# Optimization experiments

Hardware: AMD Instinct MI355X
Metric: run time of the kernel (lower is better)

Reference implementation:

```python
import jax, jax.numpy as jnp
import numpy as np
from jax import lax

N_ITERS = 20  # fixed-point iterations for the competitive-binding solve


def setup_inputs() -> dict:
    key = jax.random.key(0)
    k1, k2, k3 = jax.random.split(key, 3)
    B, nA, nB, nY = 16384, 64, 64, 1
    AT = jax.random.uniform(k1, (B, nA), dtype=jnp.float32)          # total concentrations, positive
    K_raw = jax.random.normal(k2, (nA, nB), dtype=jnp.float32)        # raw param; effective K = clamp(exp(K_raw),0,1e3)
    BT_raw = jnp.zeros((nB,), dtype=jnp.float32)                      # exp(0)=1 matches module's BT init
    W_raw = jax.random.normal(k3, (nY, nA * nB), dtype=jnp.float32)
    b_raw = jnp.zeros((nY,), dtype=jnp.float32)
    return {"AT": AT, "K_raw": K_raw, "BT_raw": BT_raw, "W_raw": W_raw, "b_raw": b_raw}


def reference(AT, K_raw, BT_raw, W_raw, b_raw):
    # parametrizations: ExpConstrain then ClampConstrain(0,1000)
    K = jnp.clip(jnp.exp(K_raw), 0.0, 1000.0)        # (nA,nB)
    BT = jnp.clip(jnp.exp(BT_raw), 0.0, 1000.0)      # (nB,)
    B = AT.shape[0]
    ATe = AT[:, :, None]                              # (B,nA,1)
    BTe = BT[None, None, :]                           # (1,1,nB), broadcasts over batch

    def one_iter(AF):
        BF = BTe / ((K * AF).sum(axis=1, keepdims=True) + 1.0)   # (B,1,nB)
        return ATe / ((K * BF).sum(axis=2, keepdims=True) + 1.0) # (B,nA,1)

    # fixed-point solve (solvers.torch_solve equivalent)
    AF = lax.fori_loop(0, N_ITERS, lambda i, a: one_iter(a), ATe)

    # mode == 'comp': extra refinement steps as written in forward
    BF = BTe / ((K * AF).sum(axis=1, keepdims=True) + 1.0)
    AF = ATe / ((K * BF).sum(axis=2, keepdims=True) + 1.0)
    BF = BTe / ((K * AF).sum(axis=1, keepdims=True) + 1.0)
    C = AF * BF * K                                   # (B,nA,nB)

    H = C.reshape(B, -1)                              # output == 'C'
    W = jnp.clip(W_raw, -10.0, 10.0)                  # linear_constrain == 'none'
    b = jnp.clip(b_raw, -10.0, 10.0)
    Y = H @ W.T + b                                   # (B,1)
    return jnp.squeeze(Y, axis=1)                     # (B,)
```

## Files before the change

### kernel.cpp

```cpp
#include <hip/hip_runtime.h>
#include <stdint.h>


typedef __attribute__((ext_vector_type(8))) short s8v;
typedef __attribute__((ext_vector_type(4))) float f4v;
typedef __attribute__((ext_vector_type(4))) unsigned u4v;

#define NPAIR 21

__device__ __forceinline__ unsigned cvtpk(float lo, float hi) {
    unsigned r;
    asm("v_cvt_pk_bf16_f32 %0, %1, %2" : "=v"(r) : "v"(lo), "v"(hi));
    return r;
}
__device__ __forceinline__ void swap32(unsigned& a, unsigned& b) {
    asm("v_permlane32_swap_b32 %0, %1" : "+v"(a), "+v"(b));
}
__device__ __forceinline__ void swap16(unsigned& a, unsigned& b) {
    asm("v_permlane16_swap_b32 %0, %1" : "+v"(a), "+v"(b));
}
__device__ __forceinline__ float clipexp(float x) {
    return fminf(__expf(x), 1000.f);
}
__device__ __forceinline__ float wclip(float x) {
    return fminf(fmaxf(x, -10.f), 10.f);
}

union FragU { unsigned u[4]; s8v s; u4v v; };

__device__ __forceinline__ s8v packB(f4v va, f4v vb) {
    unsigned a0 = cvtpk(va[0], va[1]), a1 = cvtpk(va[2], va[3]);
    unsigned b0 = cvtpk(vb[0], vb[1]), b1 = cvtpk(vb[2], vb[3]);
    swap32(a0, b0); swap16(a0, b0);
    swap32(a1, b1); swap16(a1, b1);
    FragU U; U.u[0] = a0; U.u[1] = a1; U.u[2] = b0; U.u[3] = b1;
    return U.s;
}

__global__ __launch_bounds__(64, 1)
void cn_main(const float* __restrict__ AT,
             const float* __restrict__ Kraw,
             const float* __restrict__ BTraw,
             const float* __restrict__ Wraw,
             const float* __restrict__ braw,
             float* __restrict__ out) {
    const int l  = threadIdx.x;
    const int g  = l >> 4;
    const int r  = l & 15;
    const int rb = blockIdx.x * 16;

    s8v ktA[4][2], kA[4][2], mwtA[4][2];
#pragma unroll
    for (int mt = 0; mt < 4; ++mt) {
        const int mr = mt * 16 + r;
#pragma unroll
        for (int kb = 0; kb < 2; ++kb) {
            const f4v kv0 = *reinterpret_cast<const f4v*>(Kraw + mr * 64 + kb * 32 + g * 8);
            const f4v kv1 = *reinterpret_cast<const f4v*>(Kraw + mr * 64 + kb * 32 + g * 8 + 4);
            FragU ukt, uk, umw;
#pragma unroll
            for (int w = 0; w < 4; ++w) {
                const int k0 = kb * 32 + g * 8 + 2 * w;
                const float eT0 = clipexp(Kraw[k0 * 64 + mr]);
                const float eT1 = clipexp(Kraw[(k0 + 1) * 64 + mr]);
                const float w0  = wclip(Wraw[k0 * 64 + mr]);
                const float w1  = wclip(Wraw[(k0 + 1) * 64 + mr]);
                const float eK0 = clipexp((w < 2) ? kv0[2 * w] : kv1[2 * w - 4]);
                const float eK1 = clipexp((w < 2) ? kv0[2 * w + 1] : kv1[2 * w - 3]);
                ukt.u[w] = cvtpk(eT0, eT1);
                umw.u[w] = cvtpk(eT0 * w0, eT1 * w1);
                uk.u[w]  = cvtpk(eK0, eK1);
            }
            ktA[mt][kb]  = ukt.s;
            kA[mt][kb]   = uk.s;
            mwtA[mt][kb] = umw.s;
        }
    }

    f4v bt[4];
#pragma unroll
    for (int jt = 0; jt < 4; ++jt) {
        f4v v = *reinterpret_cast<const f4v*>(BTraw + jt * 16 + g * 4);
#pragma unroll
        for (int q = 0; q < 4; ++q) bt[jt][q] = clipexp(v[q]);
    }

    f4v at[4];
#pragma unroll
    for (int it = 0; it < 4; ++it)
        at[it] = *reinterpret_cast<const f4v*>(AT + (rb + r) * 64 + it * 16 + g * 4);

    s8v afB[2];
    afB[0] = packB(at[0], at[1]);
    afB[1] = packB(at[2], at[3]);

    const f4v zero = {0.f, 0.f, 0.f, 0.f};
    const f4v ones = {1.f, 1.f, 1.f, 1.f};

#pragma unroll 1
    for (int t = 0; t < NPAIR; ++t) {
        f4v a0[4], a1[4];
#pragma unroll
        for (int jt = 0; jt < 4; ++jt)
            a0[jt] = __builtin_amdgcn_mfma_f32_16x16x32_bf16(ktA[jt][0], afB[0], ones, 0, 0, 0);
#pragma unroll
        for (int jt = 0; jt < 4; ++jt)
            a1[jt] = __builtin_amdgcn_mfma_f32_16x16x32_bf16(ktA[jt][1], afB[1], zero, 0, 0, 0);

        f4v bf0, bf1, bf2, bf3;
        {
            f4v d = a0[0] + a1[0];
#pragma unroll
            for (int q = 0; q < 4; ++q) bf0[q] = bt[0][q] * __builtin_amdgcn_rcpf(d[q]);
        }
        {
            f4v d = a0[1] + a1[1];
#pragma unroll
            for (int q = 0; q < 4; ++q) bf1[q] = bt[1][q] * __builtin_amdgcn_rcpf(d[q]);
        }
        const s8v bfB0 = packB(bf0, bf1);

        f4v c0[4];
#pragma unroll
        for (int it = 0; it < 4; ++it)
            c0[it] = __builtin_amdgcn_mfma_f32_16x16x32_bf16(kA[it][0], bfB0, ones, 0, 0, 0);

        {
            f4v d = a0[2] + a1[2];
#pragma unroll
            for (int q = 0; q < 4; ++q) bf2[q] = bt[2][q] * __builtin_amdgcn_rcpf(d[q]);
        }
        {
            f4v d = a0[3] + a1[3];
#pragma unroll
            for (int q = 0; q < 4; ++q) bf3[q] = bt[3][q] * __builtin_amdgcn_rcpf(d[q]);
        }
        const s8v bfB1 = packB(bf2, bf3);

        f4v c1[4];
#pragma unroll
        for (int it = 0; it < 4; ++it)
            c1[it] = __builtin_amdgcn_mfma_f32_16x16x32_bf16(kA[it][1], bfB1, zero, 0, 0, 0);

        f4v af[4];
#pragma unroll
        for (int it = 0; it < 4; ++it) {
            f4v d = c0[it] + c1[it];
#pragma unroll
            for (int q = 0; q < 4; ++q)
                af[it][q] = at[it][q] * __builtin_amdgcn_rcpf(d[q]);
        }
        afB[0] = packB(af[0], af[1]);
        afB[1] = packB(af[2], af[3]);
    }

    float y = 0.f;
#pragma unroll
    for (int jt = 0; jt < 4; ++jt) {
        f4v c1a, c1b, cta, ctb;
        c1a = __builtin_amdgcn_mfma_f32_16x16x32_bf16(ktA[jt][0],  afB[0], ones, 0, 0, 0);
        c1b = __builtin_amdgcn_mfma_f32_16x16x32_bf16(ktA[jt][1],  afB[1], zero, 0, 0, 0);
        cta = __builtin_amdgcn_mfma_f32_16x16x32_bf16(mwtA[jt][0], afB[0], zero, 0, 0, 0);
        ctb = __builtin_amdgcn_mfma_f32_16x16x32_bf16(mwtA[jt][1], afB[1], zero, 0, 0, 0);
        const f4v den = c1a + c1b;
        const f4v ct  = cta + ctb;
#pragma unroll
        for (int q = 0; q < 4; ++q)
            y += bt[jt][q] * __builtin_amdgcn_rcpf(den[q]) * ct[q];
    }
    y += __shfl_xor(y, 16);
    y += __shfl_xor(y, 32);

    const float bc = fminf(fmaxf(braw[0], -10.f), 10.f);
    if (l < 16) out[rb + l] = y + bc;
}

extern "C" void kernel_launch(void* const* d_in, const int* in_sizes, int n_in,
                              void* d_out, int out_size, void* d_ws, size_t ws_size,
                              hipStream_t stream) {
    (void)in_sizes; (void)n_in; (void)out_size; (void)d_ws; (void)ws_size;
    const float* AT    = (const float*)d_in[0];
    const float* Kraw  = (const float*)d_in[1];
    const float* BTraw = (const float*)d_in[2];
    const float* Wraw  = (const float*)d_in[3];
    const float* braw  = (const float*)d_in[4];

    hipLaunchKernelGGL(cn_main, dim3(16384 / 16), dim3(64), 0, stream,
                       AT, Kraw, BTraw, Wraw, braw, (float*)d_out);
}
```

Baseline: 79.36 us.

## Process two 16-row batch chunks per wavefront to interleave independent MFMA chains

Each 64-thread block now handles 32 batch rows as two independent 16-row chunks instead of one, and the grid is halved. Inside the fixed-point loop the MFMAs and reciprocal/pack steps of both chunks are interleaved, so one chunk's work can fill the dependency latency of the other. It also spreads the per-block cost of building the K, K-transpose and weighted fragments over twice as many rows. In exchange, register use per wave goes up and there are only 512 blocks, which may leave some compute units idle or underused.

```diff
diff --git a/kernel.cpp b/kernel.cpp
--- a/kernel.cpp
+++ b/kernel.cpp
@@ -47,7 +47,7 @@
     const int l  = threadIdx.x;
     const int g  = l >> 4;
     const int r  = l & 15;
-    const int rb = blockIdx.x * 16;
+    const int rb = blockIdx.x * 32;
 
     s8v ktA[4][2], kA[4][2], mwtA[4][2];
 #pragma unroll
@@ -85,94 +85,111 @@
         for (int q = 0; q < 4; ++q) bt[jt][q] = clipexp(v[q]);
     }
 
-    f4v at[4];
-#pragma unroll
-    for (int it = 0; it < 4; ++it)
-        at[it] = *reinterpret_cast<const f4v*>(AT + (rb + r) * 64 + it * 16 + g * 4);
-
-    s8v afB[2];
-    afB[0] = packB(at[0], at[1]);
-    afB[1] = packB(at[2], at[3]);
+    f4v at[2][4];
+#pragma unroll
+    for (int c = 0; c < 2; ++c)
+#pragma unroll
+        for (int it = 0; it < 4; ++it)
+            at[c][it] = *reinterpret_cast<const f4v*>(AT + (rb + c * 16 + r) * 64 + it * 16 + g * 4);
+
+    s8v afB[2][2];
+#pragma unroll
+    for (int c = 0; c < 2; ++c) {
+        afB[c][0] = packB(at[c][0], at[c][1]);
+        afB[c][1] = packB(at[c][2], at[c][3]);
+    }
 
     const f4v zero = {0.f, 0.f, 0.f, 0.f};
     const f4v ones = {1.f, 1.f, 1.f, 1.f};
 
 #pragma unroll 1
     for (int t = 0; t < NPAIR; ++t) {
-        f4v a0[4], a1[4];
-#pragma unroll
-        for (int jt = 0; jt < 4; ++jt)
-            a0[jt] = __builtin_amdgcn_mfma_f32_16x16x32_bf16(ktA[jt][0], afB[0], ones, 0, 0, 0);
-#pragma unroll
-        for (int jt = 0; jt < 4; ++jt)
-            a1[jt] = __builtin_amdgcn_mfma_f32_16x16x32_bf16(ktA[jt][1], afB[1], zero, 0, 0, 0);
-
-        f4v bf0, bf1, bf2, bf3;
-        {
-            f4v d = a0[0] + a1[0];
-#pragma unroll
-            for (int q = 0; q < 4; ++q) bf0[q] = bt[0][q] * __builtin_amdgcn_rcpf(d[q]);
-        }
-        {
-            f4v d = a0[1] + a1[1];
-#pragma unroll
-            for (int q = 0; q < 4; ++q) bf1[q] = bt[1][q] * __builtin_amdgcn_rcpf(d[q]);
-        }
-        const s8v bfB0 = packB(bf0, bf1);
-
-        f4v c0[4];
-#pragma unroll
-        for (int it = 0; it < 4; ++it)
-            c0[it] = __builtin_amdgcn_mfma_f32_16x16x32_bf16(kA[it][0], bfB0, ones, 0, 0, 0);
-
-        {
-            f4v d = a0[2] + a1[2];
-#pragma unroll
-            for (int q = 0; q < 4; ++q) bf2[q] = bt[2][q] * __builtin_amdgcn_rcpf(d[q]);
-        }
-        {
-            f4v d = a0[3] + a1[3];
-#pragma unroll
-            for (int q = 0; q < 4; ++q) bf3[q] = bt[3][q] * __builtin_amdgcn_rcpf(d[q]);
-        }
-        const s8v bfB1 = packB(bf2, bf3);
-
-        f4v c1[4];
-#pragma unroll
-        for (int it = 0; it < 4; ++it)
-            c1[it] = __builtin_amdgcn_mfma_f32_16x16x32_bf16(kA[it][1], bfB1, zero, 0, 0, 0);
-
-        f4v af[4];
-#pragma unroll
-        for (int it = 0; it < 4; ++it) {
-            f4v d = c0[it] + c1[it];
+        f4v a0[2][4], a1[2][4];
+#pragma unroll
+        for (int c = 0; c < 2; ++c)
+#pragma unroll
+            for (int jt = 0; jt < 4; ++jt)
+                a0[c][jt] = __builtin_amdgcn_mfma_f32_16x16x32_bf16(ktA[jt][0], afB[c][0], ones, 0, 0, 0);
+#pragma unroll
+        for (int c = 0; c < 2; ++c)
+#pragma unroll
+            for (int jt = 0; jt < 4; ++jt)
+                a1[c][jt] = __builtin_amdgcn_mfma_f32_16x16x32_bf16(ktA[jt][1], afB[c][1], zero, 0, 0, 0);
+
+        s8v bfB0[2], bfB1[2];
+#pragma unroll
+        for (int c = 0; c < 2; ++c) {
+            f4v bf0, bf1;
+            f4v d0 = a0[c][0] + a1[c][0];
+            f4v d1 = a0[c][1] + a1[c][1];
+#pragma unroll
+            for (int q = 0; q < 4; ++q) {
+                bf0[q] = bt[0][q] * __builtin_amdgcn_rcpf(d0[q]);
+                bf1[q] = bt[1][q] * __builtin_amdgcn_rcpf(d1[q]);
+            }
+            bfB0[c] = packB(bf0, bf1);
+        }
+        f4v c0[2][4];
+#pragma unroll
+        for (int c = 0; c < 2; ++c)
+#pragma unroll
+            for (int it = 0; it < 4; ++it)
+                c0[c][it] = __builtin_amdgcn_mfma_f32_16x16x32_bf16(kA[it][0], bfB0[c], ones, 0, 0, 0);
+#pragma unroll
+        for (int c = 0; c < 2; ++c) {
+            f4v bf2, bf3;
+            f4v d2 = a0[c][2] + a1[c][2];
+            f4v d3 = a0[c][3] + a1[c][3];
+#pragma unroll
+            for (int q = 0; q < 4; ++q) {
+                bf2[q] = bt[2][q] * __builtin_amdgcn_rcpf(d2[q]);
+                bf3[q] = bt[3][q] * __builtin_amdgcn_rcpf(d3[q]);
+            }
+            bfB1[c] = packB(bf2, bf3);
+        }
+        f4v c1v[2][4];
+#pragma unroll
+        for (int c = 0; c < 2; ++c)
+#pragma unroll
+            for (int it = 0; it < 4; ++it)
+                c1v[c][it] = __builtin_amdgcn_mfma_f32_16x16x32_bf16(kA[it][1], bfB1[c], zero, 0, 0, 0);
+
+#pragma unroll
+        for (int c = 0; c < 2; ++c) {
+            f4v af[4];
+#pragma unroll
+            for (int it = 0; it < 4; ++it) {
+                f4v d = c0[c][it] + c1v[c][it];
+#pragma unroll
+                for (int q = 0; q < 4; ++q)
+                    af[it][q] = at[c][it][q] * __builtin_amdgcn_rcpf(d[q]);
+            }
+            afB[c][0] = packB(af[0], af[1]);
+            afB[c][1] = packB(af[2], af[3]);
+        }
+    }
+
+    const float bc = fminf(fmaxf(braw[0], -10.f), 10.f);
+#pragma unroll
+    for (int c = 0; c < 2; ++c) {
+        float y = 0.f;
+#pragma unroll
+        for (int jt = 0; jt < 4; ++jt) {
+            f4v c1a, c1b, cta, ctb;
+            c1a = __builtin_amdgcn_mfma_f32_16x16x32_bf16(ktA[jt][0],  afB[c][0], ones, 0, 0, 0);
+            c1b = __builtin_amdgcn_mfma_f32_16x16x32_bf16(ktA[jt][1],  afB[c][1], zero, 0, 0, 0);
+            cta = __builtin_amdgcn_mfma_f32_16x16x32_bf16(mwtA[jt][0], afB[c][0], zero, 0, 0, 0);
+            ctb = __builtin_amdgcn_mfma_f32_16x16x32_bf16(mwtA[jt][1], afB[c][1], zero, 0, 0, 0);
+            const f4v den = c1a + c1b;
+            const f4v ct  = cta + ctb;
 #pragma unroll
             for (int q = 0; q < 4; ++q)
-                af[it][q] = at[it][q] * __builtin_amdgcn_rcpf(d[q]);
-        }
-        afB[0] = packB(af[0], af[1]);
-        afB[1] = packB(af[2], af[3]);
-    }
-
-    float y = 0.f;
-#pragma unroll
-    for (int jt = 0; jt < 4; ++jt) {
-        f4v c1a, c1b, cta, ctb;
-        c1a = __builtin_amdgcn_mfma_f32_16x16x32_bf16(ktA[jt][0],  afB[0], ones, 0, 0, 0);
-        c1b = __builtin_amdgcn_mfma_f32_16x16x32_bf16(ktA[jt][1],  afB[1], zero, 0, 0, 0);
-        cta = __builtin_amdgcn_mfma_f32_16x16x32_bf16(mwtA[jt][0], afB[0], zero, 0, 0, 0);
-        ctb = __builtin_amdgcn_mfma_f32_16x16x32_bf16(mwtA[jt][1], afB[1], zero, 0, 0, 0);
-        const f4v den = c1a + c1b;
-        const f4v ct  = cta + ctb;
-#pragma unroll
-        for (int q = 0; q < 4; ++q)
-            y += bt[jt][q] * __builtin_amdgcn_rcpf(den[q]) * ct[q];
-    }
-    y += __shfl_xor(y, 16);
-    y += __shfl_xor(y, 32);
-
-    const float bc = fminf(fmaxf(braw[0], -10.f), 10.f);
-    if (l < 16) out[rb + l] = y + bc;
+                y += bt[jt][q] * __builtin_amdgcn_rcpf(den[q]) * ct[q];
+        }
+        y += __shfl_xor(y, 16);
+        y += __shfl_xor(y, 32);
+        if (l < 16) out[rb + c * 16 + l] = y + bc;
+    }
 }
 
 extern "C" void kernel_launch(void* const* d_in, const int* in_sizes, int n_in,
@@ -185,6 +202,6 @@
     const float* Wraw  = (const float*)d_in[3];
     const float* braw  = (const float*)d_in[4];
 
-    hipLaunchKernelGGL(cn_main, dim3(16384 / 16), dim3(64), 0, stream,
+    hipLaunchKernelGGL(cn_main, dim3(16384 / 32), dim3(64), 0, stream,
                        AT, Kraw, BTraw, Wraw, braw, (float*)d_out);
 }
```

Result: slower. 85.88 us (+8.2%).
